# Kernel tuning notes

Measured on AMD Instinct MI355X. Metric: run time of the kernel, lower is better.

## Reference

```python
import jax, jax.numpy as jnp
import numpy as np

N = 100000   # nodes
E = 1200000  # edges
D = 64       # feature / hidden dim (heads=1)
L = 3        # num_layers
G = 64       # num graphs
SCALE = 1.0 / np.sqrt(D)


def setup_inputs() -> dict:
    key = jax.random.key(0)
    ks = jax.random.split(key, 12)
    inp = {
        "x": jax.random.normal(ks[0], (N, D), dtype=jnp.float32),
        "edge_index": jax.random.randint(ks[1], (2, E), 0, N, dtype=jnp.int64),
        "batch": jnp.sort(jax.random.randint(ks[2], (N,), 0, G, dtype=jnp.int64)),
        "Wq": jax.random.normal(ks[3], (L, D, D), dtype=jnp.float32) * 0.1,
        "bq": jax.random.normal(ks[4], (L, D), dtype=jnp.float32) * 0.1,
        "Wk": jax.random.normal(ks[5], (L, D, D), dtype=jnp.float32) * 0.1,
        "bk": jax.random.normal(ks[6], (L, D), dtype=jnp.float32) * 0.1,
        "Wv": jax.random.normal(ks[7], (L, D, D), dtype=jnp.float32) * 0.1,
        "bv": jax.random.normal(ks[8], (L, D), dtype=jnp.float32) * 0.1,
        "Ws": jax.random.normal(ks[9], (L, D, D), dtype=jnp.float32) * 0.1,
        "bs": jax.random.normal(ks[10], (L, D), dtype=jnp.float32) * 0.1,
    }
    return inp


def _transformer_conv(x, src, dst, Wq, bq, Wk, bk, Wv, bv, Ws, bs):
    # PyG TransformerConv, heads=1, concat=True, root_weight=True, beta=False
    q = x @ Wq + bq            # [N, D] query of target nodes
    k = x @ Wk + bk            # [N, D] key of source nodes
    v = x @ Wv + bv            # [N, D] value of source nodes
    logits = jnp.sum(q[dst] * k[src], axis=-1) * SCALE  # [E]
    # segment softmax over incoming edges of each target node
    m = jax.ops.segment_max(logits, dst, num_segments=N)        # [N]
    e = jnp.exp(logits - m[dst])                                 # [E]
    denom = jax.ops.segment_sum(e, dst, num_segments=N)         # [N]
    alpha = e / denom[dst]                                       # [E]
    agg = jax.ops.segment_sum(alpha[:, None] * v[src], dst, num_segments=N)  # [N, D]
    return agg + x @ Ws + bs   # root/skip connection


def reference(x, edge_index, batch, Wq, bq, Wk, bk, Wv, bv, Ws, bs):
    src, dst = edge_index[0], edge_index[1]
    for l in range(L):
        x = _transformer_conv(x, src, dst, Wq[l], bq[l], Wk[l], bk[l],
                              Wv[l], bv[l], Ws[l], bs[l])
        x = jax.nn.relu(x)
    # global_mean_pool
    sums = jax.ops.segment_sum(x, batch, num_segments=G)                  # [G, D]
    counts = jax.ops.segment_sum(jnp.ones((N,), x.dtype), batch, num_segments=G)
    graph_emb = sums / jnp.maximum(counts, 1.0)[:, None]
    return (x, graph_emb)
```

## Files before the change

kernel.cpp:

```cpp
#include <hip/hip_runtime.h>
#include <math.h>

#define DD 64
#define APAD 512

typedef _Float16 h2 __attribute__((ext_vector_type(2)));
typedef _Float16 h4 __attribute__((ext_vector_type(4)));
typedef _Float16 h8 __attribute__((ext_vector_type(8)));
typedef float f32x4 __attribute__((ext_vector_type(4)));

__global__ __launch_bounds__(256) void k_prep(
    const float* __restrict__ Wq, const float* __restrict__ Wk,
    const float* __restrict__ Wv, const float* __restrict__ Ws,
    _Float16* __restrict__ wf,
    const float* __restrict__ x, _Float16* __restrict__ xb,
    const int* __restrict__ dst, int* __restrict__ deg,
    unsigned short* __restrict__ pos,
    int wb, int xb_, int total8, int ecnt)
{
  int tid = threadIdx.x;
  int bid = blockIdx.x;
  if (bid < wb) {
    int id = bid * 4 + (tid >> 6);
    int lane = tid & 63;
    int layer = id >> 5;
    int c = (id >> 1) & 15;
    int s = id & 1;
    int col = c * 16 + (lane & 15);
    int mi = col >> 6;
    const float* W = (mi == 0 ? Wq : mi == 1 ? Wk : mi == 2 ? Wv : Ws)
                     + (size_t)layer * DD * DD;
    int colw = col & 63;
    _Float16* o = wf + ((((size_t)(layer * 16 + c)) * 2 + s) * 64 + lane) * 8;
    #pragma unroll
    for (int j = 0; j < 8; ++j) {
      int k = s * 32 + (lane >> 4) * 8 + j;
      o[j] = (_Float16)W[k * DD + colw];
    }
  } else if (bid < wb + xb_) {
    int i = (bid - wb) * 256 + tid;
    if (i >= total8) return;
    float4 a = ((const float4*)x)[i * 2];
    float4 b = ((const float4*)x)[i * 2 + 1];
    h8 o;
    o[0] = (_Float16)a.x; o[1] = (_Float16)a.y; o[2] = (_Float16)a.z; o[3] = (_Float16)a.w;
    o[4] = (_Float16)b.x; o[5] = (_Float16)b.y; o[6] = (_Float16)b.z; o[7] = (_Float16)b.w;
    *(h8*)(xb + (size_t)i * 8) = o;
  } else {
    int e = ((bid - wb - xb_) * 256 + tid) * 4;
    if (e + 3 < ecnt) {
      int4 d = *(const int4*)(dst + e);
      pos[e]     = (unsigned short)atomicAdd(deg + d.x, 1);
      pos[e + 1] = (unsigned short)atomicAdd(deg + d.y, 1);
      pos[e + 2] = (unsigned short)atomicAdd(deg + d.z, 1);
      pos[e + 3] = (unsigned short)atomicAdd(deg + d.w, 1);
    } else {
      for (; e < ecnt; ++e)
        pos[e] = (unsigned short)atomicAdd(deg + dst[e], 1);
    }
  }
}

#define LH_STRIDE 200
#define LS_STRIDE 72
#define WAVE_LDS  (16 * 400 + 16 * 144)

__global__ __launch_bounds__(256) void k_projM(
    const _Float16* __restrict__ xb, const _Float16* __restrict__ wf,
    const float* __restrict__ bq, const float* __restrict__ bk,
    const float* __restrict__ bv, const float* __restrict__ bs,
    _Float16* __restrict__ qh, _Float16* __restrict__ kvh,
    _Float16* __restrict__ sh, int n)
{
  __shared__ __align__(16) char lds[4 * WAVE_LDS];
  int wave = threadIdx.x >> 6;
  int lane = threadIdx.x & 63;
  int nbase = blockIdx.x * 64 + wave * 16;
  if (nbase >= n) return;

  char* wbase = lds + wave * WAVE_LDS;
  _Float16* lh = (_Float16*)wbase;
  _Float16* ls = (_Float16*)(wbase + 16 * 400);

  const int cl = lane & 15;
  const int rq = lane >> 4;

  int ar = min(nbase + cl, n - 1);
  h8 a0 = *(const h8*)(xb + (size_t)ar * DD + rq * 8);
  h8 a1 = *(const h8*)(xb + (size_t)ar * DD + 32 + rq * 8);

  #pragma unroll
  for (int c = 0; c < 16; ++c) {
    const float* bp = (c < 4) ? bq : (c < 8) ? bk : (c < 12) ? bv : bs;
    const int fb = c * 16 + rq * 4;
    float4 b4 = *(const float4*)(bp + (fb & 63));
    f32x4 acc; acc[0] = b4.x; acc[1] = b4.y; acc[2] = b4.z; acc[3] = b4.w;
    const _Float16* wp = wf + ((size_t)(c * 2) * 64 + lane) * 8;
    h8 w0 = *(const h8*)(wp);
    h8 w1 = *(const h8*)(wp + 64 * 8);
    acc = __builtin_amdgcn_mfma_f32_16x16x32_f16(w0, a0, acc, 0, 0, 0);
    acc = __builtin_amdgcn_mfma_f32_16x16x32_f16(w1, a1, acc, 0, 0, 0);

    h4 o; o[0] = (_Float16)acc[0]; o[1] = (_Float16)acc[1];
    o[2] = (_Float16)acc[2]; o[3] = (_Float16)acc[3];
    if (c < 12)
      *(h4*)(lh + cl * LH_STRIDE + fb) = o;
    else
      *(h4*)(ls + cl * LS_STRIDE + (fb - 192)) = o;
  }

  #pragma unroll
  for (int i = 0; i < 2; ++i) {
    int chunk = i * 64 + lane;
    int nd = chunk >> 3, co = chunk & 7;
    h8 v = *(const h8*)(lh + nd * LH_STRIDE + co * 8);
    if (nbase + nd < n)
      *(h8*)(qh + (size_t)(nbase + nd) * DD + co * 8) = v;
  }
  #pragma unroll
  for (int i = 0; i < 4; ++i) {
    int chunk = i * 64 + lane;
    int nd = chunk >> 4, co = chunk & 15;
    h8 v = *(const h8*)(lh + nd * LH_STRIDE + 64 + co * 8);
    if (nbase + nd < n)
      *(h8*)(kvh + (size_t)(nbase + nd) * 128 + co * 8) = v;
  }
  #pragma unroll
  for (int i = 0; i < 2; ++i) {
    int chunk = i * 64 + lane;
    int nd = chunk >> 3, co = chunk & 7;
    h8 v = *(const h8*)(ls + nd * LS_STRIDE + co * 8);
    if (nbase + nd < n)
      *(h8*)(sh + (size_t)(nbase + nd) * DD + co * 8) = v;
  }
}

__global__ __launch_bounds__(1024) void k_scanA(
    const int* __restrict__ deg, int* __restrict__ rowptr,
    int* __restrict__ btot, int* __restrict__ dbins, int n)
{
  __shared__ int wsum[16];
  __shared__ int lbin[256];
  int tid = threadIdx.x;
  int lane = tid & 63, wave = tid >> 6;
  if (tid < 256) lbin[tid] = 0;
  __syncthreads();
  int i = blockIdx.x * 4096 + tid * 4;
  int4 d = make_int4(0, 0, 0, 0);
  if (i + 3 < n) d = *(const int4*)(deg + i);
  else {
    if (i     < n) d.x = deg[i];
    if (i + 1 < n) d.y = deg[i + 1];
    if (i + 2 < n) d.z = deg[i + 2];
  }
  if (i     < n) atomicAdd(&lbin[min(d.x, 255)], 1);
  if (i + 1 < n) atomicAdd(&lbin[min(d.y, 255)], 1);
  if (i + 2 < n) atomicAdd(&lbin[min(d.z, 255)], 1);
  if (i + 3 < n) atomicAdd(&lbin[min(d.w, 255)], 1);

  int s1 = d.x, s2 = s1 + d.y, s3 = s2 + d.z, s4 = s3 + d.w;
  int s = s4;
  #pragma unroll
  for (int off = 1; off < 64; off <<= 1) {
    int t = __shfl_up(s, off);
    if (lane >= off) s += t;
  }
  if (lane == 63) wsum[wave] = s;
  __syncthreads();
  if (wave == 0) {
    int ws = (lane < 16) ? wsum[lane] : 0;
    #pragma unroll
    for (int off = 1; off < 16; off <<= 1) {
      int t = __shfl_up(ws, off);
      if (lane >= off) ws += t;
    }
    if (lane < 16) wsum[lane] = ws;
  }
  __syncthreads();
  int excl = ((wave > 0) ? wsum[wave - 1] : 0) + s - s4;
  if (i     < n) rowptr[i + 1] = excl + s1;
  if (i + 1 < n) rowptr[i + 2] = excl + s2;
  if (i + 2 < n) rowptr[i + 3] = excl + s3;
  if (i + 3 < n) rowptr[i + 4] = excl + s4;
  if (tid == 0) {
    if (blockIdx.x == 0) rowptr[0] = 0;
    btot[blockIdx.x] = wsum[15];
  }
  if (tid < 256 && lbin[tid]) atomicAdd(&dbins[tid], lbin[tid]);
}

__global__ __launch_bounds__(64) void k_scanB(
    int* __restrict__ btot, int nb, const int* __restrict__ dbins,
    int* __restrict__ dcur)
{
  int lane = threadIdx.x;
  int v = (lane < nb) ? btot[lane] : 0;
  int s = v;
  #pragma unroll
  for (int off = 1; off < 64; off <<= 1) {
    int t = __shfl_up(s, off);
    if (lane >= off) s += t;
  }
  if (lane < nb) btot[lane] = s - v;

  int4 dv = *(const int4*)(dbins + lane * 4);
  int t1 = dv.x, t2 = t1 + dv.y, t3 = t2 + dv.z, t4 = t3 + dv.w;
  int ss = t4;
  #pragma unroll
  for (int off = 1; off < 64; off <<= 1) {
    int t = __shfl_up(ss, off);
    if (lane >= off) ss += t;
  }
  int ex = ss - t4;
  dcur[lane * 4]     = ex;
  dcur[lane * 4 + 1] = ex + t1;
  dcur[lane * 4 + 2] = ex + t2;
  dcur[lane * 4 + 3] = ex + t3;
}

__global__ __launch_bounds__(1024) void k_scanCD(
    int* __restrict__ rowptr, const int* __restrict__ btot,
    const int* __restrict__ deg, int* __restrict__ dcur,
    int* __restrict__ order, int n, int nbk)
{
  __shared__ int lcnt[256];
  __shared__ int lbase[256];
  int tid = threadIdx.x;
  int b = blockIdx.x;
  if (b < nbk) {
    int off = btot[b];
    if (off) {
      int i = b * 4096 + tid * 4;
      #pragma unroll
      for (int k = 1; k <= 4; ++k)
        if (i + k <= n) rowptr[i + k] += off;
    }
  }
  if (tid < 256) lcnt[tid] = 0;
  __syncthreads();
  int i = b * 1024 + tid;
  int bin = 0, slot = 0;
  bool ok = (i < n);
  if (ok) {
    bin = min(deg[i], 255);
    slot = atomicAdd(&lcnt[bin], 1);
  }
  __syncthreads();
  if (tid < 256 && lcnt[tid]) lbase[tid] = atomicAdd(&dcur[tid], lcnt[tid]);
  __syncthreads();
  if (ok) order[(n - 1) - (lbase[bin] + slot)] = i;
}

__global__ __launch_bounds__(256) void k_fill(
    const int* __restrict__ src, const int* __restrict__ dst,
    const int* __restrict__ rowptr, const unsigned short* __restrict__ pos,
    int* __restrict__ adj, int ecnt)
{
  int e = (blockIdx.x * 256 + threadIdx.x) * 4;
  if (e + 3 < ecnt) {
    int4 d = *(const int4*)(dst + e);
    int4 s = *(const int4*)(src + e);
    ushort4 p = *(const ushort4*)(pos + e);
    adj[rowptr[d.x] + p.x] = s.x;
    adj[rowptr[d.y] + p.y] = s.y;
    adj[rowptr[d.z] + p.z] = s.z;
    adj[rowptr[d.w] + p.w] = s.w;
  } else {
    for (; e < ecnt; ++e)
      adj[rowptr[dst[e]] + pos[e]] = src[e];
  }
}

#define H2OF(v, i) __builtin_shufflevector((v), (v), 2*(i), 2*(i)+1)

template<bool LAST>
__global__ __launch_bounds__(256) void k_node(
    const _Float16* __restrict__ qh, const _Float16* __restrict__ kvh,
    const int* __restrict__ rowptr, const int* __restrict__ adj,
    const int* __restrict__ order,
    const _Float16* __restrict__ sh, float* __restrict__ outp,
    _Float16* __restrict__ xbnext, int n)
{
  int wid = (blockIdx.x * blockDim.x + threadIdx.x) >> 6;
  int lane = threadIdx.x & 63;
  const int g = lane >> 3;
  const int t = lane & 7;

  int idx = wid * 8 + g;
  bool nok = (idx < n);
  int node = order[nok ? idx : (n - 1)];

  const h8 q8 = *(const h8*)(qh + (size_t)node * DD + t * 8);
  const h2 qp0 = H2OF(q8, 0), qp1 = H2OF(q8, 1), qp2 = H2OF(q8, 2), qp3 = H2OF(q8, 3);

  const int e0 = rowptr[node];
  const int d  = nok ? (rowptr[node + 1] - e0) : 0;

  float mg = -1e30f, den = 0.f;
  float agg[8] = {0.f, 0.f, 0.f, 0.f, 0.f, 0.f, 0.f, 0.f};

  const char* kvb = (const char*)kvh;
  const unsigned tb = (unsigned)t << 4;

  h8 kP, vP;
  {
    int s = adj[e0];
    unsigned off = ((unsigned)s << 8) + tb;
    kP = *(const h8*)(kvb + off);
    vP = *(const h8*)(kvb + off + 128);
  }

  for (int it = 0; it < d; ++it) {
    const h8 kc = kP, vc = vP;
    {
      int s2 = adj[e0 + it + 1];
      unsigned off = ((unsigned)s2 << 8) + tb;
      kP = *(const h8*)(kvb + off);
      vP = *(const h8*)(kvb + off + 128);
    }

#if __has_builtin(__builtin_amdgcn_fdot2)
    float p = __builtin_amdgcn_fdot2(qp0, H2OF(kc, 0), 0.f, false);
    p = __builtin_amdgcn_fdot2(qp1, H2OF(kc, 1), p, false);
    p = __builtin_amdgcn_fdot2(qp2, H2OF(kc, 2), p, false);
    p = __builtin_amdgcn_fdot2(qp3, H2OF(kc, 3), p, false);
#else
    h2 ph = qp0 * H2OF(kc, 0);
    ph = qp1 * H2OF(kc, 1) + ph;
    ph = qp2 * H2OF(kc, 2) + ph;
    ph = qp3 * H2OF(kc, 3) + ph;
    float p = (float)ph.x + (float)ph.y;
#endif
    p += __shfl_xor(p, 1);
    p += __shfl_xor(p, 2);
    p += __shfl_xor(p, 4);
    p *= 0.125f;

    if (p > mg) {
      float c = __expf(mg - p);
      den *= c;
      #pragma unroll
      for (int j = 0; j < 8; ++j) agg[j] *= c;
      mg = p;
    }
    float w = __expf(p - mg);
    den += w;
    #pragma unroll
    for (int j = 0; j < 8; ++j)
      agg[j] = fmaf(w, (float)vc[j], agg[j]);
  }

  if (nok) {
    float inv = (den > 0.f) ? (1.0f / den) : 0.f;
    const h8 s8 = *(const h8*)(sh + (size_t)node * DD + t * 8);
    float r[8];
    #pragma unroll
    for (int j = 0; j < 8; ++j)
      r[j] = fmaxf(fmaf(agg[j], inv, (float)s8[j]), 0.f);
    if (LAST) {
      float* op = outp + (size_t)node * DD + t * 8;
      *(float4*)(op)     = make_float4(r[0], r[1], r[2], r[3]);
      *(float4*)(op + 4) = make_float4(r[4], r[5], r[6], r[7]);
    } else {
      h8 xh;
      #pragma unroll
      for (int j = 0; j < 8; ++j) xh[j] = (_Float16)r[j];
      *(h8*)(xbnext + (size_t)node * DD + t * 8) = xh;
    }
  }
}

__global__ __launch_bounds__(64) void k_pool_sum(
    const float* __restrict__ x, const int* __restrict__ batch,
    float* __restrict__ gsum, int n)
{
  int lane = threadIdx.x;
  int n0 = blockIdx.x * 64;
  if (n0 >= n) return;
  int n1 = min(n0 + 64, n);
  float acc = 0.f;
  int g_prev = batch[n0];
  for (int nn = n0; nn < n1; ++nn) {
    int g = batch[nn];
    if (g != g_prev) {
      atomicAdd(gsum + (size_t)g_prev * DD + lane, acc);
      acc = 0.f; g_prev = g;
    }
    acc += x[(size_t)nn * DD + lane];
  }
  atomicAdd(gsum + (size_t)g_prev * DD + lane, acc);
}

__device__ __forceinline__ int lbound(const int* __restrict__ a, int n, int key)
{
  int lo = 0, hi = n;
  while (lo < hi) {
    int mid = (lo + hi) >> 1;
    if (a[mid] < key) lo = mid + 1; else hi = mid;
  }
  return lo;
}

__global__ __launch_bounds__(256) void k_pool_div(
    const float* __restrict__ gsum, const int* __restrict__ batch,
    float* __restrict__ emb, int gtot, int n)
{
  int gid = blockIdx.x * blockDim.x + threadIdx.x;
  if (gid >= gtot * DD) return;
  int g = gid >> 6;
  int cnt = lbound(batch, n, g + 1) - lbound(batch, n, g);
  emb[gid] = gsum[gid] / fmaxf((float)cnt, 1.0f);
}

extern "C" void kernel_launch(void* const* d_in, const int* in_sizes, int n_in,
                              void* d_out, int out_size, void* d_ws, size_t ws_size,
                              hipStream_t stream)
{
  const float* x_in  = (const float*)d_in[0];
  const int*   ei    = (const int*)  d_in[1];
  const int*   batch = (const int*)  d_in[2];
  const float* Wq = (const float*)d_in[3];
  const float* bq = (const float*)d_in[4];
  const float* Wk = (const float*)d_in[5];
  const float* bk = (const float*)d_in[6];
  const float* Wv = (const float*)d_in[7];
  const float* bv = (const float*)d_in[8];
  const float* Ws = (const float*)d_in[9];
  const float* bs = (const float*)d_in[10];

  const int nd     = in_sizes[0];
  const int n      = nd / DD;
  const int ecnt   = in_sizes[1] / 2;
  const int layers = in_sizes[3] / (DD * DD);
  const int gtot   = (out_size - nd) / DD;

  const int* src = ei;
  const int* dst = ei + ecnt;

  char* cur = (char*)d_ws;
  _Float16*  SH  = (_Float16*)cur;  cur += (size_t)nd * 2;
  _Float16*  XB  = (_Float16*)cur;  cur += (size_t)nd * 2;
  _Float16*  QH  = (_Float16*)cur;  cur += (size_t)nd * 2;
  _Float16*  KVH = (_Float16*)cur;  cur += (size_t)nd * 4;
  _Float16*  WF  = (_Float16*)cur;  cur += (size_t)layers * 16384 * 2;
  int* rowptr = (int*)cur;          cur += (size_t)(n + 4) * 4;
  int* adj    = (int*)cur;          cur += (size_t)(ecnt + APAD) * 4;
  int* deg    = (int*)cur;          cur += (size_t)n * 4;
  int* dbins  = (int*)cur;          cur += 256 * 4;
  float* gsum = (float*)cur;        cur += (size_t)gtot * DD * 4;
  int* dcur   = (int*)cur;          cur += 256 * 4;
  int* btot   = (int*)cur;          cur += 64 * 4;
  int* order  = (int*)cur;          cur += (size_t)n * 4;
  unsigned short* pos = (unsigned short*)cur; cur += (size_t)ecnt * 2;

  float* out = (float*)d_out;

  hipMemsetAsync(adj + ecnt, 0,
                 (size_t)(APAD + n + 256 + gtot * DD) * 4, stream);

  const int wb  = layers * 8;
  const int xbk = (n * 8 + 255) / 256;
  const int hbk = (ecnt + 1023) / 1024;
  k_prep<<<wb + xbk + hbk, 256, 0, stream>>>(Wq, Wk, Wv, Ws, WF,
                                             x_in, XB, dst, deg, pos,
                                             wb, xbk, n * 8, ecnt);
  const int nbk = (n + 4095) / 4096;
  k_scanA<<<nbk, 1024, 0, stream>>>(deg, rowptr, btot, dbins, n);
  k_scanB<<<1, 64, 0, stream>>>(btot, nbk, dbins, dcur);
  const int dblk = (n + 1023) / 1024;
  k_scanCD<<<dblk, 1024, 0, stream>>>(rowptr, btot, deg, dcur, order, n, nbk);
  k_fill<<<hbk, 256, 0, stream>>>(src, dst, rowptr, pos, adj, ecnt);

  const int pj = (n + 63) / 64;
  const int nb = (n + 31) / 32;

  for (int l = 0; l < layers; ++l) {
    const size_t bo = (size_t)l * DD;
    k_projM<<<pj, 256, 0, stream>>>(XB, WF + (size_t)l * 16384,
                                    bq + bo, bk + bo, bv + bo, bs + bo,
                                    QH, KVH, SH, n);
    if (l == layers - 1)
      k_node<true><<<nb, 256, 0, stream>>>(QH, KVH, rowptr, adj, order,
                                           SH, out, XB, n);
    else
      k_node<false><<<nb, 256, 0, stream>>>(QH, KVH, rowptr, adj, order,
                                            SH, out, XB, n);
  }

  const int pbk = (n + 63) / 64;
  k_pool_sum<<<pbk, 64, 0, stream>>>(out, batch, gsum, n);
  const int fb = (gtot * DD + 255) / 256;
  k_pool_div<<<fb, 256, 0, stream>>>(gsum, batch, out + (size_t)nd, gtot, n);
}
```

Before: 334.5 us.

## Privatize degree histogram into eight copies to reduce atomic contention

Edge-degree counting now spreads its atomics across eight per-copy degree arrays chosen by block index, and tags each edge's slot with its copy id in the upper bits of the 16-bit position. The scan kernel then folds the copies into per-copy base offsets and a total degree, which the fill kernel uses to place each edge. The aim is to reduce same-address atomic contention on high-degree destination nodes, at the cost of more memset, scan traffic and an extra gather in the fill step. The histogram blocks also move to the front of the prep grid so they are scheduled first. Per-copy slots must fit in 13 bits.

```diff
diff --git a/kernel.cpp b/kernel.cpp
--- a/kernel.cpp
+++ b/kernel.cpp
@@ -3,6 +3,7 @@
 
 #define DD 64
 #define APAD 512
+#define NCOPY 8
 
 typedef _Float16 h2 __attribute__((ext_vector_type(2)));
 typedef _Float16 h4 __attribute__((ext_vector_type(4)));
@@ -14,14 +15,35 @@
     const float* __restrict__ Wv, const float* __restrict__ Ws,
     _Float16* __restrict__ wf,
     const float* __restrict__ x, _Float16* __restrict__ xb,
-    const int* __restrict__ dst, int* __restrict__ deg,
+    const int* __restrict__ dst, int* __restrict__ degp,
     unsigned short* __restrict__ pos,
-    int wb, int xb_, int total8, int ecnt)
+    int hb, int wb, int total8, int ecnt, int n)
 {
   int tid = threadIdx.x;
   int bid = blockIdx.x;
-  if (bid < wb) {
-    int id = bid * 4 + (tid >> 6);
+  if (bid < hb) {
+    const int c = bid & (NCOPY - 1);
+    int* dp = degp + (size_t)c * n;
+    const unsigned ctag = (unsigned)c << 13;
+    int e = (bid * 256 + tid) * 4;
+    if (e + 3 < ecnt) {
+      int4 d = *(const int4*)(dst + e);
+      unsigned s0 = atomicAdd(dp + d.x, 1);
+      unsigned s1 = atomicAdd(dp + d.y, 1);
+      unsigned s2 = atomicAdd(dp + d.z, 1);
+      unsigned s3 = atomicAdd(dp + d.w, 1);
+      ushort4 pv;
+      pv.x = (unsigned short)(ctag | s0);
+      pv.y = (unsigned short)(ctag | s1);
+      pv.z = (unsigned short)(ctag | s2);
+      pv.w = (unsigned short)(ctag | s3);
+      *(ushort4*)(pos + e) = pv;
+    } else {
+      for (; e < ecnt; ++e)
+        pos[e] = (unsigned short)(ctag | atomicAdd(dp + dst[e], 1));
+    }
+  } else if (bid < hb + wb) {
+    int id = (bid - hb) * 4 + (tid >> 6);
     int lane = tid & 63;
     int layer = id >> 5;
     int c = (id >> 1) & 15;
@@ -37,8 +59,8 @@
       int k = s * 32 + (lane >> 4) * 8 + j;
       o[j] = (_Float16)W[k * DD + colw];
     }
-  } else if (bid < wb + xb_) {
-    int i = (bid - wb) * 256 + tid;
+  } else {
+    int i = (bid - hb - wb) * 256 + tid;
     if (i >= total8) return;
     float4 a = ((const float4*)x)[i * 2];
     float4 b = ((const float4*)x)[i * 2 + 1];
@@ -46,18 +68,6 @@
     o[0] = (_Float16)a.x; o[1] = (_Float16)a.y; o[2] = (_Float16)a.z; o[3] = (_Float16)a.w;
     o[4] = (_Float16)b.x; o[5] = (_Float16)b.y; o[6] = (_Float16)b.z; o[7] = (_Float16)b.w;
     *(h8*)(xb + (size_t)i * 8) = o;
-  } else {
-    int e = ((bid - wb - xb_) * 256 + tid) * 4;
-    if (e + 3 < ecnt) {
-      int4 d = *(const int4*)(dst + e);
-      pos[e]     = (unsigned short)atomicAdd(deg + d.x, 1);
-      pos[e + 1] = (unsigned short)atomicAdd(deg + d.y, 1);
-      pos[e + 2] = (unsigned short)atomicAdd(deg + d.z, 1);
-      pos[e + 3] = (unsigned short)atomicAdd(deg + d.w, 1);
-    } else {
-      for (; e < ecnt; ++e)
-        pos[e] = (unsigned short)atomicAdd(deg + dst[e], 1);
-    }
   }
 }
 
@@ -136,7 +146,8 @@
 }
 
 __global__ __launch_bounds__(1024) void k_scanA(
-    const int* __restrict__ deg, int* __restrict__ rowptr,
+    const int* __restrict__ degp, int* __restrict__ basep,
+    int* __restrict__ degt, int* __restrict__ rowptr,
     int* __restrict__ btot, int* __restrict__ dbins, int n)
 {
   __shared__ int wsum[16];
@@ -146,24 +157,46 @@
   if (tid < 256) lbin[tid] = 0;
   __syncthreads();
   int i = blockIdx.x * 4096 + tid * 4;
-  int4 d = make_int4(0, 0, 0, 0);
-  if (i + 3 < n) d = *(const int4*)(deg + i);
-  else {
-    if (i     < n) d.x = deg[i];
-    if (i + 1 < n) d.y = deg[i + 1];
-    if (i + 2 < n) d.z = deg[i + 2];
-  }
-  if (i     < n) atomicAdd(&lbin[min(d.x, 255)], 1);
-  if (i + 1 < n) atomicAdd(&lbin[min(d.y, 255)], 1);
-  if (i + 2 < n) atomicAdd(&lbin[min(d.z, 255)], 1);
-  if (i + 3 < n) atomicAdd(&lbin[min(d.w, 255)], 1);
-
-  int s1 = d.x, s2 = s1 + d.y, s3 = s2 + d.z, s4 = s3 + d.w;
+
+  int4 t = make_int4(0, 0, 0, 0);
+  if (i + 3 < n) {
+    int4 run = make_int4(0, 0, 0, 0);
+    #pragma unroll
+    for (int x = 0; x < NCOPY; ++x) {
+      int4 v = *(const int4*)(degp + (size_t)x * n + i);
+      *(int4*)(basep + (size_t)x * n + i) = run;
+      run.x += v.x; run.y += v.y; run.z += v.z; run.w += v.w;
+    }
+    t = run;
+    *(int4*)(degt + i) = t;
+  } else {
+    for (int k = 0; k < 4; ++k) {
+      int ii = i + k;
+      if (ii < n) {
+        int run = 0;
+        #pragma unroll
+        for (int x = 0; x < NCOPY; ++x) {
+          int v = degp[(size_t)x * n + ii];
+          basep[(size_t)x * n + ii] = run;
+          run += v;
+        }
+        (&t.x)[k] = run;
+        degt[ii] = run;
+      }
+    }
+  }
+
+  if (i     < n) atomicAdd(&lbin[min(t.x, 255)], 1);
+  if (i + 1 < n) atomicAdd(&lbin[min(t.y, 255)], 1);
+  if (i + 2 < n) atomicAdd(&lbin[min(t.z, 255)], 1);
+  if (i + 3 < n) atomicAdd(&lbin[min(t.w, 255)], 1);
+
+  int s1 = t.x, s2 = s1 + t.y, s3 = s2 + t.z, s4 = s3 + t.w;
   int s = s4;
   #pragma unroll
   for (int off = 1; off < 64; off <<= 1) {
-    int t = __shfl_up(s, off);
-    if (lane >= off) s += t;
+    int tt = __shfl_up(s, off);
+    if (lane >= off) s += tt;
   }
   if (lane == 63) wsum[wave] = s;
   __syncthreads();
@@ -171,8 +204,8 @@
     int ws = (lane < 16) ? wsum[lane] : 0;
     #pragma unroll
     for (int off = 1; off < 16; off <<= 1) {
-      int t = __shfl_up(ws, off);
-      if (lane >= off) ws += t;
+      int tt = __shfl_up(ws, off);
+      if (lane >= off) ws += tt;
     }
     if (lane < 16) wsum[lane] = ws;
   }
@@ -220,7 +253,7 @@
 
 __global__ __launch_bounds__(1024) void k_scanCD(
     int* __restrict__ rowptr, const int* __restrict__ btot,
-    const int* __restrict__ deg, int* __restrict__ dcur,
+    const int* __restrict__ degt, int* __restrict__ dcur,
     int* __restrict__ order, int n, int nbk)
 {
   __shared__ int lcnt[256];
@@ -242,7 +275,7 @@
   int bin = 0, slot = 0;
   bool ok = (i < n);
   if (ok) {
-    bin = min(deg[i], 255);
+    bin = min(degt[i], 255);
     slot = atomicAdd(&lcnt[bin], 1);
   }
   __syncthreads();
@@ -253,21 +286,25 @@
 
 __global__ __launch_bounds__(256) void k_fill(
     const int* __restrict__ src, const int* __restrict__ dst,
-    const int* __restrict__ rowptr, const unsigned short* __restrict__ pos,
-    int* __restrict__ adj, int ecnt)
+    const int* __restrict__ rowptr, const int* __restrict__ basep,
+    const unsigned short* __restrict__ pos,
+    int* __restrict__ adj, int ecnt, int n)
 {
   int e = (blockIdx.x * 256 + threadIdx.x) * 4;
   if (e + 3 < ecnt) {
     int4 d = *(const int4*)(dst + e);
     int4 s = *(const int4*)(src + e);
     ushort4 p = *(const ushort4*)(pos + e);
-    adj[rowptr[d.x] + p.x] = s.x;
-    adj[rowptr[d.y] + p.y] = s.y;
-    adj[rowptr[d.z] + p.z] = s.z;
-    adj[rowptr[d.w] + p.w] = s.w;
+    adj[rowptr[d.x] + basep[(size_t)(p.x >> 13) * n + d.x] + (p.x & 8191)] = s.x;
+    adj[rowptr[d.y] + basep[(size_t)(p.y >> 13) * n + d.y] + (p.y & 8191)] = s.y;
+    adj[rowptr[d.z] + basep[(size_t)(p.z >> 13) * n + d.z] + (p.z & 8191)] = s.z;
+    adj[rowptr[d.w] + basep[(size_t)(p.w >> 13) * n + d.w] + (p.w & 8191)] = s.w;
   } else {
-    for (; e < ecnt; ++e)
-      adj[rowptr[dst[e]] + pos[e]] = src[e];
+    for (; e < ecnt; ++e) {
+      int d = dst[e];
+      unsigned short p = pos[e];
+      adj[rowptr[d] + basep[(size_t)(p >> 13) * n + d] + (p & 8191)] = src[e];
+    }
   }
 }
 
@@ -445,9 +482,11 @@
   _Float16*  WF  = (_Float16*)cur;  cur += (size_t)layers * 16384 * 2;
   int* rowptr = (int*)cur;          cur += (size_t)(n + 4) * 4;
   int* adj    = (int*)cur;          cur += (size_t)(ecnt + APAD) * 4;
-  int* deg    = (int*)cur;          cur += (size_t)n * 4;
+  int* degp   = (int*)cur;          cur += (size_t)NCOPY * n * 4;
   int* dbins  = (int*)cur;          cur += 256 * 4;
   float* gsum = (float*)cur;        cur += (size_t)gtot * DD * 4;
+  int* basep  = (int*)cur;          cur += (size_t)NCOPY * n * 4;
+  int* degt   = (int*)cur;          cur += (size_t)n * 4;
   int* dcur   = (int*)cur;          cur += 256 * 4;
   int* btot   = (int*)cur;          cur += 64 * 4;
   int* order  = (int*)cur;          cur += (size_t)n * 4;
@@ -456,20 +495,20 @@
   float* out = (float*)d_out;
 
   hipMemsetAsync(adj + ecnt, 0,
-                 (size_t)(APAD + n + 256 + gtot * DD) * 4, stream);
-
+                 (size_t)(APAD + NCOPY * n + 256 + gtot * DD) * 4, stream);
+
+  const int hbk = (ecnt + 1023) / 1024;
   const int wb  = layers * 8;
   const int xbk = (n * 8 + 255) / 256;
-  const int hbk = (ecnt + 1023) / 1024;
-  k_prep<<<wb + xbk + hbk, 256, 0, stream>>>(Wq, Wk, Wv, Ws, WF,
-                                             x_in, XB, dst, deg, pos,
-                                             wb, xbk, n * 8, ecnt);
+  k_prep<<<hbk + wb + xbk, 256, 0, stream>>>(Wq, Wk, Wv, Ws, WF,
+                                             x_in, XB, dst, degp, pos,
+                                             hbk, wb, n * 8, ecnt, n);
   const int nbk = (n + 4095) / 4096;
-  k_scanA<<<nbk, 1024, 0, stream>>>(deg, rowptr, btot, dbins, n);
+  k_scanA<<<nbk, 1024, 0, stream>>>(degp, basep, degt, rowptr, btot, dbins, n);
   k_scanB<<<1, 64, 0, stream>>>(btot, nbk, dbins, dcur);
   const int dblk = (n + 1023) / 1024;
-  k_scanCD<<<dblk, 1024, 0, stream>>>(rowptr, btot, deg, dcur, order, n, nbk);
-  k_fill<<<hbk, 256, 0, stream>>>(src, dst, rowptr, pos, adj, ecnt);
+  k_scanCD<<<dblk, 1024, 0, stream>>>(rowptr, btot, degt, dcur, order, n, nbk);
+  k_fill<<<hbk, 256, 0, stream>>>(src, dst, rowptr, basep, pos, adj, ecnt, n);
 
   const int pj = (n + 63) / 64;
   const int nb = (n + 31) / 32;
```

Result: no change. 332.3 us (-0.7%).

## Restructure CSR build launches and fuse adjacency fill with first projection

Applied to the files above, without the earlier changes.

Splits the edge histogram into its own kernel and merges the degree scan into the weight/feature conversion kernel, using 1024-node scan blocks with a two-segment block-total scan. The CSR adjacency fill is fused with the layer-0 projection in one launch, so independent work shares a grid and one launch per layer-0 projection is dropped. The cost is more blocks in the scan pass and a larger LDS footprint for the fill blocks, which could lower their occupancy. The btot buffer grows to 128 entries to cover up to 128 scan blocks.

```diff
diff --git a/kernel.cpp b/kernel.cpp
--- a/kernel.cpp
+++ b/kernel.cpp
@@ -9,19 +9,86 @@
 typedef _Float16 h8 __attribute__((ext_vector_type(8)));
 typedef float f32x4 __attribute__((ext_vector_type(4)));
 
-__global__ __launch_bounds__(256) void k_prep(
+__global__ __launch_bounds__(256) void k_hist(
+    const int* __restrict__ dst, int* __restrict__ deg,
+    unsigned short* __restrict__ pos, int ecnt)
+{
+  int e = (blockIdx.x * 256 + threadIdx.x) * 4;
+  if (e + 3 < ecnt) {
+    int4 d = *(const int4*)(dst + e);
+    ushort4 pv;
+    pv.x = (unsigned short)atomicAdd(deg + d.x, 1);
+    pv.y = (unsigned short)atomicAdd(deg + d.y, 1);
+    pv.z = (unsigned short)atomicAdd(deg + d.z, 1);
+    pv.w = (unsigned short)atomicAdd(deg + d.w, 1);
+    *(ushort4*)(pos + e) = pv;
+  } else {
+    for (; e < ecnt; ++e)
+      pos[e] = (unsigned short)atomicAdd(deg + dst[e], 1);
+  }
+}
+
+__global__ __launch_bounds__(256) void k_mix(
     const float* __restrict__ Wq, const float* __restrict__ Wk,
     const float* __restrict__ Wv, const float* __restrict__ Ws,
     _Float16* __restrict__ wf,
     const float* __restrict__ x, _Float16* __restrict__ xb,
-    const int* __restrict__ dst, int* __restrict__ deg,
-    unsigned short* __restrict__ pos,
-    int wb, int xb_, int total8, int ecnt)
+    const int* __restrict__ deg, int* __restrict__ rowptr,
+    int* __restrict__ btot, int* __restrict__ dbins,
+    int nbk, int wb, int total8, int n)
 {
   int tid = threadIdx.x;
   int bid = blockIdx.x;
-  if (bid < wb) {
-    int id = bid * 4 + (tid >> 6);
+  if (bid < nbk) {
+    __shared__ int wsum[4];
+    __shared__ int lbin[256];
+    int lane = tid & 63, wave = tid >> 6;
+    lbin[tid] = 0;
+    __syncthreads();
+    int i = bid * 1024 + tid * 4;
+    int4 d = make_int4(0, 0, 0, 0);
+    if (i + 3 < n) d = *(const int4*)(deg + i);
+    else {
+      if (i     < n) d.x = deg[i];
+      if (i + 1 < n) d.y = deg[i + 1];
+      if (i + 2 < n) d.z = deg[i + 2];
+    }
+    if (i     < n) atomicAdd(&lbin[min(d.x, 255)], 1);
+    if (i + 1 < n) atomicAdd(&lbin[min(d.y, 255)], 1);
+    if (i + 2 < n) atomicAdd(&lbin[min(d.z, 255)], 1);
+    if (i + 3 < n) atomicAdd(&lbin[min(d.w, 255)], 1);
+
+    int s1 = d.x, s2 = s1 + d.y, s3 = s2 + d.z, s4 = s3 + d.w;
+    int s = s4;
+    #pragma unroll
+    for (int off = 1; off < 64; off <<= 1) {
+      int t = __shfl_up(s, off);
+      if (lane >= off) s += t;
+    }
+    if (lane == 63) wsum[wave] = s;
+    __syncthreads();
+    if (wave == 0) {
+      int ws = (lane < 4) ? wsum[lane] : 0;
+      #pragma unroll
+      for (int off = 1; off < 4; off <<= 1) {
+        int t = __shfl_up(ws, off);
+        if (lane >= off) ws += t;
+      }
+      if (lane < 4) wsum[lane] = ws;
+    }
+    __syncthreads();
+    int excl = ((wave > 0) ? wsum[wave - 1] : 0) + s - s4;
+    if (i     < n) rowptr[i + 1] = excl + s1;
+    if (i + 1 < n) rowptr[i + 2] = excl + s2;
+    if (i + 2 < n) rowptr[i + 3] = excl + s3;
+    if (i + 3 < n) rowptr[i + 4] = excl + s4;
+    if (tid == 0) {
+      if (bid == 0) rowptr[0] = 0;
+      btot[bid] = wsum[3];
+    }
+    if (lbin[tid]) atomicAdd(&dbins[tid], lbin[tid]);
+  } else if (bid < nbk + wb) {
+    int id = (bid - nbk) * 4 + (tid >> 6);
     int lane = tid & 63;
     int layer = id >> 5;
     int c = (id >> 1) & 15;
@@ -37,8 +104,8 @@
       int k = s * 32 + (lane >> 4) * 8 + j;
       o[j] = (_Float16)W[k * DD + colw];
     }
-  } else if (bid < wb + xb_) {
-    int i = (bid - wb) * 256 + tid;
+  } else {
+    int i = (bid - nbk - wb) * 256 + tid;
     if (i >= total8) return;
     float4 a = ((const float4*)x)[i * 2];
     float4 b = ((const float4*)x)[i * 2 + 1];
@@ -46,36 +113,88 @@
     o[0] = (_Float16)a.x; o[1] = (_Float16)a.y; o[2] = (_Float16)a.z; o[3] = (_Float16)a.w;
     o[4] = (_Float16)b.x; o[5] = (_Float16)b.y; o[6] = (_Float16)b.z; o[7] = (_Float16)b.w;
     *(h8*)(xb + (size_t)i * 8) = o;
-  } else {
-    int e = ((bid - wb - xb_) * 256 + tid) * 4;
-    if (e + 3 < ecnt) {
-      int4 d = *(const int4*)(dst + e);
-      pos[e]     = (unsigned short)atomicAdd(deg + d.x, 1);
-      pos[e + 1] = (unsigned short)atomicAdd(deg + d.y, 1);
-      pos[e + 2] = (unsigned short)atomicAdd(deg + d.z, 1);
-      pos[e + 3] = (unsigned short)atomicAdd(deg + d.w, 1);
-    } else {
-      for (; e < ecnt; ++e)
-        pos[e] = (unsigned short)atomicAdd(deg + dst[e], 1);
-    }
-  }
+  }
+}
+
+__global__ __launch_bounds__(64) void k_scanB(
+    int* __restrict__ btot, int nb, const int* __restrict__ dbins,
+    int* __restrict__ dcur)
+{
+  int lane = threadIdx.x;
+  int v0 = (lane < nb) ? btot[lane] : 0;
+  int v1 = (64 + lane < nb) ? btot[64 + lane] : 0;
+  int s0 = v0;
+  #pragma unroll
+  for (int off = 1; off < 64; off <<= 1) {
+    int t = __shfl_up(s0, off);
+    if (lane >= off) s0 += t;
+  }
+  int tot0 = __shfl(s0, 63);
+  int s1 = v1;
+  #pragma unroll
+  for (int off = 1; off < 64; off <<= 1) {
+    int t = __shfl_up(s1, off);
+    if (lane >= off) s1 += t;
+  }
+  if (lane < nb) btot[lane] = s0 - v0;
+  if (64 + lane < nb) btot[64 + lane] = tot0 + s1 - v1;
+
+  int4 dv = *(const int4*)(dbins + lane * 4);
+  int t1 = dv.x, t2 = t1 + dv.y, t3 = t2 + dv.z, t4 = t3 + dv.w;
+  int ss = t4;
+  #pragma unroll
+  for (int off = 1; off < 64; off <<= 1) {
+    int t = __shfl_up(ss, off);
+    if (lane >= off) ss += t;
+  }
+  int ex = ss - t4;
+  dcur[lane * 4]     = ex;
+  dcur[lane * 4 + 1] = ex + t1;
+  dcur[lane * 4 + 2] = ex + t2;
+  dcur[lane * 4 + 3] = ex + t3;
+}
+
+__global__ __launch_bounds__(1024) void k_scanCD(
+    int* __restrict__ rowptr, const int* __restrict__ btot,
+    const int* __restrict__ deg, int* __restrict__ dcur,
+    int* __restrict__ order, int n)
+{
+  __shared__ int lcnt[256];
+  __shared__ int lbase[256];
+  int tid = threadIdx.x;
+  int b = blockIdx.x;
+  int off = btot[b];
+  int i = b * 1024 + tid;
+  if (off && i < n) rowptr[i + 1] += off;
+  if (tid < 256) lcnt[tid] = 0;
+  __syncthreads();
+  int bin = 0, slot = 0;
+  bool ok = (i < n);
+  if (ok) {
+    bin = min(deg[i], 255);
+    slot = atomicAdd(&lcnt[bin], 1);
+  }
+  __syncthreads();
+  if (tid < 256 && lcnt[tid]) lbase[tid] = atomicAdd(&dcur[tid], lcnt[tid]);
+  __syncthreads();
+  if (ok) order[(n - 1) - (lbase[bin] + slot)] = i;
 }
 
 #define LH_STRIDE 200
 #define LS_STRIDE 72
 #define WAVE_LDS  (16 * 400 + 16 * 144)
 
-__global__ __launch_bounds__(256) void k_projM(
+__device__ __forceinline__ void projM_body(
+    int blk, int tid, char* lds,
     const _Float16* __restrict__ xb, const _Float16* __restrict__ wf,
     const float* __restrict__ bq, const float* __restrict__ bk,
     const float* __restrict__ bv, const float* __restrict__ bs,
     _Float16* __restrict__ qh, _Float16* __restrict__ kvh,
     _Float16* __restrict__ sh, int n)
 {
-  __shared__ __align__(16) char lds[4 * WAVE_LDS];
-  int wave = threadIdx.x >> 6;
-  int lane = threadIdx.x & 63;
-  int nbase = blockIdx.x * 64 + wave * 16;
+  int wave = tid >> 6;
+  int lane = tid & 63;
+  int nbase = blk * 64 + wave * 16;
   if (nbase >= n) return;
 
   char* wbase = lds + wave * WAVE_LDS;
@@ -135,139 +254,47 @@
   }
 }
 
-__global__ __launch_bounds__(1024) void k_scanA(
-    const int* __restrict__ deg, int* __restrict__ rowptr,
-    int* __restrict__ btot, int* __restrict__ dbins, int n)
-{
-  __shared__ int wsum[16];
-  __shared__ int lbin[256];
-  int tid = threadIdx.x;
-  int lane = tid & 63, wave = tid >> 6;
-  if (tid < 256) lbin[tid] = 0;
-  __syncthreads();
-  int i = blockIdx.x * 4096 + tid * 4;
-  int4 d = make_int4(0, 0, 0, 0);
-  if (i + 3 < n) d = *(const int4*)(deg + i);
-  else {
-    if (i     < n) d.x = deg[i];
-    if (i + 1 < n) d.y = deg[i + 1];
-    if (i + 2 < n) d.z = deg[i + 2];
-  }
-  if (i     < n) atomicAdd(&lbin[min(d.x, 255)], 1);
-  if (i + 1 < n) atomicAdd(&lbin[min(d.y, 255)], 1);
-  if (i + 2 < n) atomicAdd(&lbin[min(d.z, 255)], 1);
-  if (i + 3 < n) atomicAdd(&lbin[min(d.w, 255)], 1);
-
-  int s1 = d.x, s2 = s1 + d.y, s3 = s2 + d.z, s4 = s3 + d.w;
-  int s = s4;
-  #pragma unroll
-  for (int off = 1; off < 64; off <<= 1) {
-    int t = __shfl_up(s, off);
-    if (lane >= off) s += t;
-  }
-  if (lane == 63) wsum[wave] = s;
-  __syncthreads();
-  if (wave == 0) {
-    int ws = (lane < 16) ? wsum[lane] : 0;
-    #pragma unroll
-    for (int off = 1; off < 16; off <<= 1) {
-      int t = __shfl_up(ws, off);
-      if (lane >= off) ws += t;
-    }
-    if (lane < 16) wsum[lane] = ws;
-  }
-  __syncthreads();
-  int excl = ((wave > 0) ? wsum[wave - 1] : 0) + s - s4;
-  if (i     < n) rowptr[i + 1] = excl + s1;
-  if (i + 1 < n) rowptr[i + 2] = excl + s2;
-  if (i + 2 < n) rowptr[i + 3] = excl + s3;
-  if (i + 3 < n) rowptr[i + 4] = excl + s4;
-  if (tid == 0) {
-    if (blockIdx.x == 0) rowptr[0] = 0;
-    btot[blockIdx.x] = wsum[15];
-  }
-  if (tid < 256 && lbin[tid]) atomicAdd(&dbins[tid], lbin[tid]);
-}
-
-__global__ __launch_bounds__(64) void k_scanB(
-    int* __restrict__ btot, int nb, const int* __restrict__ dbins,
-    int* __restrict__ dcur)
-{
-  int lane = threadIdx.x;
-  int v = (lane < nb) ? btot[lane] : 0;
-  int s = v;
-  #pragma unroll
-  for (int off = 1; off < 64; off <<= 1) {
-    int t = __shfl_up(s, off);
-    if (lane >= off) s += t;
-  }
-  if (lane < nb) btot[lane] = s - v;
-
-  int4 dv = *(const int4*)(dbins + lane * 4);
-  int t1 = dv.x, t2 = t1 + dv.y, t3 = t2 + dv.z, t4 = t3 + dv.w;
-  int ss = t4;
-  #pragma unroll
-  for (int off = 1; off < 64; off <<= 1) {
-    int t = __shfl_up(ss, off);
-    if (lane >= off) ss += t;
-  }
-  int ex = ss - t4;
-  dcur[lane * 4]     = ex;
-  dcur[lane * 4 + 1] = ex + t1;
-  dcur[lane * 4 + 2] = ex + t2;
-  dcur[lane * 4 + 3] = ex + t3;
-}
-
-__global__ __launch_bounds__(1024) void k_scanCD(
-    int* __restrict__ rowptr, const int* __restrict__ btot,
-    const int* __restrict__ deg, int* __restrict__ dcur,
-    int* __restrict__ order, int n, int nbk)
-{
-  __shared__ int lcnt[256];
-  __shared__ int lbase[256];
-  int tid = threadIdx.x;
-  int b = blockIdx.x;
-  if (b < nbk) {
-    int off = btot[b];
-    if (off) {
-      int i = b * 4096 + tid * 4;
-      #pragma unroll
-      for (int k = 1; k <= 4; ++k)
-        if (i + k <= n) rowptr[i + k] += off;
-    }
-  }
-  if (tid < 256) lcnt[tid] = 0;
-  __syncthreads();
-  int i = b * 1024 + tid;
-  int bin = 0, slot = 0;
-  bool ok = (i < n);
-  if (ok) {
-    bin = min(deg[i], 255);
-    slot = atomicAdd(&lcnt[bin], 1);
-  }
-  __syncthreads();
-  if (tid < 256 && lcnt[tid]) lbase[tid] = atomicAdd(&dcur[tid], lcnt[tid]);
-  __syncthreads();
-  if (ok) order[(n - 1) - (lbase[bin] + slot)] = i;
-}
-
-__global__ __launch_bounds__(256) void k_fill(
+__global__ __launch_bounds__(256) void k_projM(
+    const _Float16* __restrict__ xb, const _Float16* __restrict__ wf,
+    const float* __restrict__ bq, const float* __restrict__ bk,
+    const float* __restrict__ bv, const float* __restrict__ bs,
+    _Float16* __restrict__ qh, _Float16* __restrict__ kvh,
+    _Float16* __restrict__ sh, int n)
+{
+  __shared__ __align__(16) char lds[4 * WAVE_LDS];
+  projM_body(blockIdx.x, threadIdx.x, lds, xb, wf, bq, bk, bv, bs,
+             qh, kvh, sh, n);
+}
+
+__global__ __launch_bounds__(256) void k_fillproj(
     const int* __restrict__ src, const int* __restrict__ dst,
     const int* __restrict__ rowptr, const unsigned short* __restrict__ pos,
-    int* __restrict__ adj, int ecnt)
-{
-  int e = (blockIdx.x * 256 + threadIdx.x) * 4;
-  if (e + 3 < ecnt) {
-    int4 d = *(const int4*)(dst + e);
-    int4 s = *(const int4*)(src + e);
-    ushort4 p = *(const ushort4*)(pos + e);
-    adj[rowptr[d.x] + p.x] = s.x;
-    adj[rowptr[d.y] + p.y] = s.y;
-    adj[rowptr[d.z] + p.z] = s.z;
-    adj[rowptr[d.w] + p.w] = s.w;
+    int* __restrict__ adj, int ecnt, int hbk,
+    const _Float16* __restrict__ xb, const _Float16* __restrict__ wf,
+    const float* __restrict__ bq, const float* __restrict__ bk,
+    const float* __restrict__ bv, const float* __restrict__ bs,
+    _Float16* __restrict__ qh, _Float16* __restrict__ kvh,
+    _Float16* __restrict__ sh, int n)
+{
+  __shared__ __align__(16) char lds[4 * WAVE_LDS];
+  int bid = blockIdx.x;
+  if (bid < hbk) {
+    int e = (bid * 256 + threadIdx.x) * 4;
+    if (e + 3 < ecnt) {
+      int4 d = *(const int4*)(dst + e);
+      int4 s = *(const int4*)(src + e);
+      ushort4 p = *(const ushort4*)(pos + e);
+      adj[rowptr[d.x] + p.x] = s.x;
+      adj[rowptr[d.y] + p.y] = s.y;
+      adj[rowptr[d.z] + p.z] = s.z;
+      adj[rowptr[d.w] + p.w] = s.w;
+    } else {
+      for (; e < ecnt; ++e)
+        adj[rowptr[dst[e]] + pos[e]] = src[e];
+    }
   } else {
-    for (; e < ecnt; ++e)
-      adj[rowptr[dst[e]] + pos[e]] = src[e];
+    projM_body(bid - hbk, threadIdx.x, lds, xb, wf, bq, bk, bv, bs,
+               qh, kvh, sh, n);
   }
 }
 
@@ -449,7 +476,7 @@
   int* dbins  = (int*)cur;          cur += 256 * 4;
   float* gsum = (float*)cur;        cur += (size_t)gtot * DD * 4;
   int* dcur   = (int*)cur;          cur += 256 * 4;
-  int* btot   = (int*)cur;          cur += 64 * 4;
+  int* btot   = (int*)cur;          cur += 128 * 4;
   int* order  = (int*)cur;          cur += (size_t)n * 4;
   unsigned short* pos = (unsigned short*)cur; cur += (size_t)ecnt * 2;
 
@@ -458,27 +485,30 @@
   hipMemsetAsync(adj + ecnt, 0,
                  (size_t)(APAD + n + 256 + gtot * DD) * 4, stream);
 
+  const int hbk = (ecnt + 1023) / 1024;
+  const int nbk = (n + 1023) / 1024;
   const int wb  = layers * 8;
   const int xbk = (n * 8 + 255) / 256;
-  const int hbk = (ecnt + 1023) / 1024;
-  k_prep<<<wb + xbk + hbk, 256, 0, stream>>>(Wq, Wk, Wv, Ws, WF,
-                                             x_in, XB, dst, deg, pos,
-                                             wb, xbk, n * 8, ecnt);
-  const int nbk = (n + 4095) / 4096;
-  k_scanA<<<nbk, 1024, 0, stream>>>(deg, rowptr, btot, dbins, n);
+  const int pj  = (n + 63) / 64;
+  const int nb  = (n + 31) / 32;
+
+  k_hist<<<hbk, 256, 0, stream>>>(dst, deg, pos, ecnt);
+  k_mix<<<nbk + wb + xbk, 256, 0, stream>>>(Wq, Wk, Wv, Ws, WF, x_in, XB,
+                                            deg, rowptr, btot, dbins,
+                                            nbk, wb, n * 8, n);
   k_scanB<<<1, 64, 0, stream>>>(btot, nbk, dbins, dcur);
-  const int dblk = (n + 1023) / 1024;
-  k_scanCD<<<dblk, 1024, 0, stream>>>(rowptr, btot, deg, dcur, order, n, nbk);
-  k_fill<<<hbk, 256, 0, stream>>>(src, dst, rowptr, pos, adj, ecnt);
-
-  const int pj = (n + 63) / 64;
-  const int nb = (n + 31) / 32;
-
+  k_scanCD<<<nbk, 1024, 0, stream>>>(rowptr, btot, deg, dcur, order, n);
+
+  k_fillproj<<<hbk + pj, 256, 0, stream>>>(src, dst, rowptr, pos, adj, ecnt,
+                                           hbk, XB, WF, bq, bk, bv, bs,
+                                           QH, KVH, SH, n);
   for (int l = 0; l < layers; ++l) {
-    const size_t bo = (size_t)l * DD;
-    k_projM<<<pj, 256, 0, stream>>>(XB, WF + (size_t)l * 16384,
-                                    bq + bo, bk + bo, bv + bo, bs + bo,
-                                    QH, KVH, SH, n);
+    if (l > 0) {
+      const size_t bo = (size_t)l * DD;
+      k_projM<<<pj, 256, 0, stream>>>(XB, WF + (size_t)l * 16384,
+                                      bq + bo, bk + bo, bv + bo, bs + bo,
+                                      QH, KVH, SH, n);
+    }
     if (l == layers - 1)
       k_node<true><<<nb, 256, 0, stream>>>(QH, KVH, rowptr, adj, order,
                                            SH, out, XB, n);
```

Measured after the change: 322.2 us. 1.04x faster.
